# Performance work log

Measured on AMD Instinct MI355X. Metric: run time of the kernel, lower is better.

## Reference

```python
import jax, jax.numpy as jnp
import numpy as np

EPS = 1e-6


def softmax_kernel_transformation(data, is_query, projection_matrix):
    # data: [B,L,H,D], projection_matrix: [M,D]
    d = data.shape[-1]
    m = projection_matrix.shape[0]
    data_normalizer = 1.0 / jnp.sqrt(jnp.sqrt(jnp.float32(d)))
    data = data_normalizer * data
    ratio = 1.0 / jnp.sqrt(jnp.float32(m))
    data_dash = jnp.einsum('blhd,md->blhm', data, projection_matrix)
    diag_data = jnp.sum(jnp.square(data), axis=-1, keepdims=True) / 2.0  # [B,L,H,1]
    if is_query:
        stab = jnp.max(data_dash, axis=-1, keepdims=True)  # per-position max over M
    else:
        stab = jnp.max(data_dash, axis=(1, 3), keepdims=True)  # max over L and M
    return ratio * (jnp.exp(data_dash - diag_data - stab) + EPS)


def causal_linear_attention(qp, kp, v):
    # qp,kp: [L,B,H,M]; v: [L,B,H,D]. Sequential prefix-sum recurrence (FAVOR+ causal).
    B, H, M = qp.shape[1], qp.shape[2], qp.shape[3]
    D = v.shape[-1]
    kv0 = jnp.zeros((B, H, M, D), dtype=v.dtype)
    ks0 = jnp.zeros((B, H, M), dtype=kp.dtype)

    def step(carry, inp):
        kv_sum, k_sum = carry
        q_t, k_t, v_t = inp  # [B,H,M], [B,H,M], [B,H,D]
        kv_sum = kv_sum + jnp.einsum('bhm,bhd->bhmd', k_t, v_t)
        k_sum = k_sum + k_t
        num_t = jnp.einsum('bhmd,bhm->bhd', kv_sum, q_t)  # numerator row
        den_t = jnp.einsum('bhm,bhm->bh', q_t, k_sum)     # normalizer row
        return (kv_sum, k_sum), (num_t, den_t)

    (_, _), (num, den) = jax.lax.scan(step, (kv0, ks0), (qp, kp, v))
    return num, den  # [L,B,H,D], [L,B,H]


def favor_attention(query, key, value, projection_matrix):
    query_prime = softmax_kernel_transformation(query, True, projection_matrix)   # [B,L,H,M]
    key_prime = softmax_kernel_transformation(key, False, projection_matrix)      # [B,L,H,M]
    qp = jnp.transpose(query_prime, (1, 0, 2, 3))  # [L,B,H,M]
    kp = jnp.transpose(key_prime, (1, 0, 2, 3))
    v = jnp.transpose(value, (1, 0, 2, 3))         # [L,B,H,D]
    num, den = causal_linear_attention(qp, kp, v)
    av = jnp.transpose(num, (1, 0, 2, 3))          # [B,L,H,D]
    norm = jnp.transpose(den, (1, 0, 2))[..., None]  # [B,L,H,1]
    return av / norm


def setup_inputs() -> dict:
    B, L, H, D, M = 2, 2048, 8, 64, 128
    root = jax.random.key(0)
    kq, kk, kv, kp = jax.random.split(root, 4)
    return {
        'query': jax.random.normal(kq, (B, L, H, D), dtype=jnp.float32),
        'key': jax.random.normal(kk, (B, L, H, D), dtype=jnp.float32),
        'value': jax.random.normal(kv, (B, L, H, D), dtype=jnp.float32),
        'projection_matrix': jax.random.normal(kp, (M, D), dtype=jnp.float32),
    }


def reference(query, key, value, projection_matrix):
    return favor_attention(query, key, value, projection_matrix)
```

## Files before the change

kernel.cpp:

```cpp
#include <hip/hip_runtime.h>
#include <math.h>

typedef __attribute__((ext_vector_type(8))) short short8;
typedef __attribute__((ext_vector_type(4))) float f32x4;
typedef __attribute__((ext_vector_type(4))) unsigned short u16x4;

constexpr int B_ = 2, L_ = 2048, H_ = 8, D_ = 64, M_ = 128;
constexpr int T_ = 64;
constexpr int C_ = L_ / T_;
constexpr float DN_ = 0.35355339059327373f;
constexpr float RATIO_ = 0.08838834764831845f;
constexpr float EPSV_ = 1e-6f;
constexpr float REPS_ = RATIO_ * EPSV_;
constexpr float KEPS_ = 64.0f * REPS_;

constexpr int XQH_ = 0, XQL_ = 4608, XKH_ = 9216, XKL_ = 13824;
constexpr int PHO_ = 18432, PLO_ = 27648;
constexpr int QPST_ = 0, VTO_ = 9216, KPTO_ = 18432, KVSTO_ = 27648;

__device__ inline unsigned short f2bf(float x) {
  const unsigned u = __float_as_uint(x);
  return (unsigned short)((u + 0x7fffu + ((u >> 16) & 1u)) >> 16);
}
__device__ inline float bf2f(unsigned short h) {
  return __uint_as_float(((unsigned)h) << 16);
}

__global__ __launch_bounds__(256, 2) void feat_kernel(
    const float* __restrict__ q, const float* __restrict__ k,
    const float* __restrict__ P, const float* __restrict__ v,
    unsigned short* __restrict__ qp16, unsigned short* __restrict__ kp16,
    unsigned short* __restrict__ kvc16, float* __restrict__ ksc,
    unsigned short* __restrict__ vt16, float* __restrict__ blockmax,
    float* __restrict__ vsum) {
  __shared__ __align__(16) unsigned short sm[36864];
  __shared__ float diagq_s[T_];
  __shared__ float diagk_s[T_];
  __shared__ float wred_s[2][T_];
  __shared__ float red4_s[4];

  const int sub = blockIdx.x;
  const int c = sub % C_, bh = sub / C_;
  const int b = bh >> 3, h = bh & 7;
  const int tid = threadIdx.x;
  const int w = tid >> 6, lane = tid & 63;
  const int l15 = lane & 15, l16 = lane >> 4;
  const int rblk = (w >> 1) * 32, cblk = (w & 1) * 64;

  f32x4 vreg[4];
#pragma unroll
  for (int it = 0; it < 4; ++it) {
    const int i4 = tid + 256 * it;
    const int r = i4 >> 4, d0 = (i4 & 15) * 4;
    vreg[it] = *reinterpret_cast<const f32x4*>(
        &v[((size_t)(b * L_ + c * T_ + r) * H_ + h) * D_ + d0]);
  }

#define STAGE_X(xptr, XB, LB, dg)                                             \
  _Pragma("unroll") for (int it = 0; it < 4; ++it) {                          \
    const int i4 = tid + 256 * it;                                            \
    const int r = i4 >> 4, d0 = (i4 & 15) * 4;                                \
    f32x4 t4 = *reinterpret_cast<const f32x4*>(                               \
        &(xptr)[((size_t)(b * L_ + c * T_ + r) * H_ + h) * D_ + d0]);         \
    u16x4 hi, lo;                                                             \
    float sq = 0.f;                                                           \
    _Pragma("unroll") for (int j = 0; j < 4; ++j) {                           \
      const float xv = t4[j] * DN_;                                           \
      sq += xv * xv;                                                          \
      const unsigned short hb = f2bf(xv);                                     \
      hi[j] = hb;                                                             \
      lo[j] = f2bf(xv - bf2f(hb));                                            \
    }                                                                         \
    *reinterpret_cast<u16x4*>(&sm[(XB) + r * 72 + d0]) = hi;                  \
    *reinterpret_cast<u16x4*>(&sm[(LB) + r * 72 + d0]) = lo;                  \
    _Pragma("unroll") for (int off = 1; off < 16; off <<= 1)                  \
        sq += __shfl_xor(sq, off, 64);                                        \
    if ((tid & 15) == 0) (dg)[r] = sq;                                        \
  }

#define DASH_MFMA(accv, XB, LB)                                               \
  _Pragma("unroll") for (int kk = 0; kk < 2; ++kk) {                          \
    short8 ah[2], al[2], bh8[4], bl8[4];                                      \
    _Pragma("unroll") for (int ti = 0; ti < 2; ++ti) {                        \
      ah[ti] = *reinterpret_cast<const short8*>(                              \
          &sm[(XB) + (rblk + ti * 16 + l15) * 72 + kk * 32 + l16 * 8]);       \
      al[ti] = *reinterpret_cast<const short8*>(                              \
          &sm[(LB) + (rblk + ti * 16 + l15) * 72 + kk * 32 + l16 * 8]);       \
    }                                                                         \
    _Pragma("unroll") for (int tj = 0; tj < 4; ++tj) {                        \
      bh8[tj] = *reinterpret_cast<const short8*>(                             \
          &sm[PHO_ + (cblk + tj * 16 + l15) * 72 + kk * 32 + l16 * 8]);       \
      bl8[tj] = *reinterpret_cast<const short8*>(                             \
          &sm[PLO_ + (cblk + tj * 16 + l15) * 72 + kk * 32 + l16 * 8]);       \
    }                                                                         \
    _Pragma("unroll") for (int ti = 0; ti < 2; ++ti)                          \
        _Pragma("unroll") for (int tj = 0; tj < 4; ++tj) {                    \
      accv[ti][tj] = __builtin_amdgcn_mfma_f32_16x16x32_bf16(                 \
          al[ti], bh8[tj], accv[ti][tj], 0, 0, 0);                            \
      accv[ti][tj] = __builtin_amdgcn_mfma_f32_16x16x32_bf16(                 \
          ah[ti], bl8[tj], accv[ti][tj], 0, 0, 0);                            \
      accv[ti][tj] = __builtin_amdgcn_mfma_f32_16x16x32_bf16(                 \
          ah[ti], bh8[tj], accv[ti][tj], 0, 0, 0);                            \
    }                                                                         \
  }

  STAGE_X(q, XQH_, XQL_, diagq_s);
  STAGE_X(k, XKH_, XKL_, diagk_s);
  for (int i4 = tid; i4 < M_ * 16; i4 += 256) {
    const int m = i4 >> 4, d0 = (i4 & 15) * 4;
    const f32x4 t4 = *reinterpret_cast<const f32x4*>(&P[m * D_ + d0]);
    u16x4 hi, lo;
#pragma unroll
    for (int j = 0; j < 4; ++j) {
      hi[j] = f2bf(t4[j]);
      lo[j] = f2bf(t4[j] - bf2f(hi[j]));
    }
    *reinterpret_cast<u16x4*>(&sm[PHO_ + m * 72 + d0]) = hi;
    *reinterpret_cast<u16x4*>(&sm[PLO_ + m * 72 + d0]) = lo;
  }
  __syncthreads();

  f32x4 accq[2][4];
#pragma unroll
  for (int i = 0; i < 2; ++i)
#pragma unroll
    for (int j = 0; j < 4; ++j) accq[i][j] = {0.f, 0.f, 0.f, 0.f};
  DASH_MFMA(accq, XQH_, XQL_);

  {
    float rmax[2][4];
#pragma unroll
    for (int ti = 0; ti < 2; ++ti)
#pragma unroll
      for (int j = 0; j < 4; ++j) {
        float m0 = fmaxf(fmaxf(accq[ti][0][j], accq[ti][1][j]),
                         fmaxf(accq[ti][2][j], accq[ti][3][j]));
#pragma unroll
        for (int off = 1; off < 16; off <<= 1)
          m0 = fmaxf(m0, __shfl_xor(m0, off, 64));
        rmax[ti][j] = m0;
      }
    if (l15 == 0) {
#pragma unroll
      for (int ti = 0; ti < 2; ++ti)
#pragma unroll
        for (int j = 0; j < 4; ++j)
          wred_s[w & 1][rblk + ti * 16 + l16 * 4 + j] = rmax[ti][j];
    }
  }
  __syncthreads();

  f32x4 acck[2][4];
#pragma unroll
  for (int i = 0; i < 2; ++i)
#pragma unroll
    for (int j = 0; j < 4; ++j) acck[i][j] = {0.f, 0.f, 0.f, 0.f};
  DASH_MFMA(acck, XKH_, XKL_);
  {
    float bm = -INFINITY;
#pragma unroll
    for (int ti = 0; ti < 2; ++ti)
#pragma unroll
      for (int tj = 0; tj < 4; ++tj)
#pragma unroll
        for (int j = 0; j < 4; ++j) bm = fmaxf(bm, acck[ti][tj][j]);
#pragma unroll
    for (int off = 1; off < 64; off <<= 1)
      bm = fmaxf(bm, __shfl_xor(bm, off, 64));
    if (lane == 0) red4_s[w] = bm;
  }
#pragma unroll
  for (int ti = 0; ti < 2; ++ti)
#pragma unroll
    for (int j = 0; j < 4; ++j) {
      const int row = rblk + ti * 16 + l16 * 4 + j;
      const float sub2 =
          0.5f * diagq_s[row] + fmaxf(wred_s[0][row], wred_s[1][row]);
#pragma unroll
      for (int tj = 0; tj < 4; ++tj) {
        const int col = cblk + tj * 16 + l15;
        sm[QPST_ + row * 136 + col] =
            f2bf(RATIO_ * (expf(accq[ti][tj][j] - sub2) + EPSV_));
      }
    }
  __syncthreads();

  {
    unsigned short* outr = qp16 + ((size_t)bh * L_ + c * T_) * M_;
    for (int i8 = tid; i8 < T_ * 16; i8 += 256) {
      const int row = i8 >> 4, m0 = (i8 & 15) * 8;
      *reinterpret_cast<short8*>(&outr[row * M_ + m0]) =
          *reinterpret_cast<const short8*>(&sm[QPST_ + row * 136 + m0]);
    }
  }
  const float lmax =
      fmaxf(fmaxf(red4_s[0], red4_s[1]), fmaxf(red4_s[2], red4_s[3]));
  if (tid == 0) blockmax[sub] = lmax;

  {
    unsigned short* kpr = kp16 + ((size_t)bh * L_ + c * T_) * M_;
#pragma unroll
    for (int ti = 0; ti < 2; ++ti)
#pragma unroll
      for (int j = 0; j < 4; ++j) {
        const int row = rblk + ti * 16 + l16 * 4 + j;
        const float sub2 = 0.5f * diagk_s[row] + lmax;
#pragma unroll
        for (int tj = 0; tj < 4; ++tj) {
          const int col = cblk + tj * 16 + l15;
          const unsigned short us = f2bf(RATIO_ * expf(acck[ti][tj][j] - sub2));
          kpr[row * M_ + col] = us;
          sm[KPTO_ + col * 72 + row] = us;
        }
      }
  }
#pragma unroll
  for (int it = 0; it < 4; ++it) {
    const int i4 = tid + 256 * it;
    const int t = i4 >> 4, d0 = (i4 & 15) * 4;
#pragma unroll
    for (int j = 0; j < 4; ++j) sm[VTO_ + (d0 + j) * 72 + t] = f2bf(vreg[it][j]);
  }
  __syncthreads();

  {
    unsigned short* vg = vt16 + (size_t)(bh * C_ + c) * (D_ * T_);
    for (int i8 = tid; i8 < D_ * 8; i8 += 256) {
      const int d = i8 >> 3, t0 = (i8 & 7) * 8;
      *reinterpret_cast<short8*>(&vg[d * T_ + t0]) =
          *reinterpret_cast<const short8*>(&sm[VTO_ + d * 72 + t0]);
    }
  }
  if (tid < M_) {
    float s = 0.f;
#pragma unroll
    for (int t8 = 0; t8 < 8; ++t8) {
      const short8 h8 =
          *reinterpret_cast<const short8*>(&sm[KPTO_ + tid * 72 + t8 * 8]);
#pragma unroll
      for (int j = 0; j < 8; ++j) s += bf2f((unsigned short)h8[j]);
    }
    ksc[(size_t)(bh * C_ + c) * M_ + tid] = s;
  }
  if (tid >= 128 && tid < 128 + D_) {
    const int d = tid - 128;
    float s = 0.f;
#pragma unroll
    for (int t8 = 0; t8 < 8; ++t8) {
      const short8 h8 =
          *reinterpret_cast<const short8*>(&sm[VTO_ + d * 72 + t8 * 8]);
#pragma unroll
      for (int j = 0; j < 8; ++j) s += bf2f((unsigned short)h8[j]);
    }
    vsum[(size_t)(bh * C_ + c) * D_ + d] = s;
  }
  f32x4 acc2[2][4];
#pragma unroll
  for (int i = 0; i < 2; ++i)
#pragma unroll
    for (int j = 0; j < 4; ++j) acc2[i][j] = {0.f, 0.f, 0.f, 0.f};
#pragma unroll
  for (int kk = 0; kk < 2; ++kk) {
    short8 av[2], bv[4];
#pragma unroll
    for (int ti = 0; ti < 2; ++ti)
      av[ti] = *reinterpret_cast<const short8*>(
          &sm[VTO_ + (rblk + ti * 16 + l15) * 72 + kk * 32 + l16 * 8]);
#pragma unroll
    for (int tj = 0; tj < 4; ++tj)
      bv[tj] = *reinterpret_cast<const short8*>(
          &sm[KPTO_ + (cblk + tj * 16 + l15) * 72 + kk * 32 + l16 * 8]);
#pragma unroll
    for (int ti = 0; ti < 2; ++ti)
#pragma unroll
      for (int tj = 0; tj < 4; ++tj)
        acc2[ti][tj] = __builtin_amdgcn_mfma_f32_16x16x32_bf16(
            av[ti], bv[tj], acc2[ti][tj], 0, 0, 0);
  }
#pragma unroll
  for (int ti = 0; ti < 2; ++ti)
#pragma unroll
    for (int j = 0; j < 4; ++j) {
      const int row = rblk + ti * 16 + l16 * 4 + j;
#pragma unroll
      for (int tj = 0; tj < 4; ++tj) {
        const int col = cblk + tj * 16 + l15;
        sm[KVSTO_ + row * 136 + col] = f2bf(acc2[ti][tj][j]);
      }
    }
  __syncthreads();
  {
    unsigned short* ob = kvc16 + (size_t)(bh * C_ + c) * (M_ * D_);
    for (int i8 = tid; i8 < D_ * 16; i8 += 256) {
      const int d = i8 >> 4, m0 = (i8 & 15) * 8;
      *reinterpret_cast<short8*>(&ob[d * M_ + m0]) =
          *reinterpret_cast<const short8*>(&sm[KVSTO_ + d * 136 + m0]);
    }
  }
#undef STAGE_X
#undef DASH_MFMA
}

__global__ __launch_bounds__(256) void prefix_kernel(
    const unsigned short* __restrict__ kvc16,
    unsigned short* __restrict__ kvp16, float* __restrict__ ksc,
    const float* __restrict__ blockmax, const float* __restrict__ vsum) {
  __shared__ float bm_s[C_];
  __shared__ float sc_s[C_];
  __shared__ float vs_s[2][C_];
  const int bid = blockIdx.x;
  const int ej = bid & 31, bh = bid >> 5;
  if (threadIdx.x < C_) bm_s[threadIdx.x] = blockmax[bh * C_ + threadIdx.x];
  if (threadIdx.x >= 64 && threadIdx.x < 64 + 2 * C_) {
    const int t = threadIdx.x - 64;
    const int ld = t >> 5, cc = t & 31;
    vs_s[ld][cc] = vsum[(size_t)(bh * C_ + cc) * D_ + ej * 2 + ld];
  }
  __syncthreads();
  if (threadIdx.x < C_) {
    float km = -INFINITY;
#pragma unroll
    for (int cc = 0; cc < C_; ++cc) km = fmaxf(km, bm_s[cc]);
    sc_s[threadIdx.x] = expf(bm_s[threadIdx.x] - km);
  }
  __syncthreads();
  const int e = ej * 256 + threadIdx.x;
  const int dl = threadIdx.x >> 7;
  float vals[C_];
#pragma unroll
  for (int cc = 0; cc < C_; ++cc)
    vals[cc] = bf2f(kvc16[(size_t)(bh * C_ + cc) * (M_ * D_) + e]) * sc_s[cc] +
               REPS_ * vs_s[dl][cc];
  float run = 0.f;
#pragma unroll
  for (int cc = 0; cc < C_; ++cc) {
    const float t = vals[cc];
    vals[cc] = run;
    run += t;
  }
#pragma unroll
  for (int cc = 0; cc < C_; ++cc)
    kvp16[(size_t)(bh * C_ + cc) * (M_ * D_) + e] = f2bf(vals[cc]);
  if (ej == 0 && threadIdx.x < M_) {
    const int m = threadIdx.x;
    float ks[C_];
#pragma unroll
    for (int cc = 0; cc < C_; ++cc)
      ks[cc] = ksc[(size_t)(bh * C_ + cc) * M_ + m] * sc_s[cc] + KEPS_;
    float rs = 0.f;
#pragma unroll
    for (int cc = 0; cc < C_; ++cc) {
      const float t = ks[cc];
      ks[cc] = rs;
      rs += t;
    }
#pragma unroll
    for (int cc = 0; cc < C_; ++cc)
      ksc[(size_t)(bh * C_ + cc) * M_ + m] = ks[cc];
  }
}

__global__ __launch_bounds__(256, 3) void intra_kernel(
    const unsigned short* __restrict__ qp16,
    const unsigned short* __restrict__ kp16,
    const unsigned short* __restrict__ vt16,
    const unsigned short* __restrict__ kvp16, const float* __restrict__ ksp,
    const float* __restrict__ blockmax, float* __restrict__ out) {
  __shared__ __align__(16) unsigned short qp_s[T_][136];
  __shared__ __align__(16) unsigned short kp_s[T_][136];
  __shared__ __align__(16) unsigned short S_s[T_][72];
  __shared__ float ksp_s[M_];
  __shared__ float denp_s[4][T_];
  __shared__ float den_s[T_];
  __shared__ float qsum_s[T_];
  __shared__ float bm_s[C_];

  const int bid = blockIdx.x;
  const int c = bid % C_, bh = bid / C_;
  const int b = bh >> 3, h = bh & 7;
  const int tid = threadIdx.x;
  const int w = tid >> 6, lane = tid & 63;
  const int l15 = lane & 15, l16 = lane >> 4;
  const int dblk = (w & 1) * 32;

  const unsigned short* qpt = qp16 + ((size_t)bh * L_ + c * T_) * M_;
  const unsigned short* kpt = kp16 + ((size_t)bh * L_ + c * T_) * M_;
  const unsigned short* kvt = kvp16 + (size_t)(bh * C_ + c) * (M_ * D_);
  const unsigned short* vg = vt16 + (size_t)(bh * C_ + c) * (D_ * T_);

  short8 vtr[2][2], kvr[4][2];
#pragma unroll
  for (int kk = 0; kk < 2; ++kk)
#pragma unroll
    for (int tj = 0; tj < 2; ++tj)
      vtr[kk][tj] = *reinterpret_cast<const short8*>(
          &vg[(dblk + tj * 16 + l15) * T_ + kk * 32 + l16 * 8]);
#pragma unroll
  for (int kk = 0; kk < 4; ++kk)
#pragma unroll
    for (int tj = 0; tj < 2; ++tj)
      kvr[kk][tj] = *reinterpret_cast<const short8*>(
          &kvt[(dblk + tj * 16 + l15) * M_ + kk * 32 + l16 * 8]);

  if (tid < C_) bm_s[tid] = blockmax[bh * C_ + tid];
  for (int i8 = tid; i8 < T_ * 16; i8 += 256) {
    const int r = i8 >> 4, m0 = (i8 & 15) * 8;
    *reinterpret_cast<short8*>(&qp_s[r][m0]) =
        *reinterpret_cast<const short8*>(&qpt[r * M_ + m0]);
    *reinterpret_cast<short8*>(&kp_s[r][m0]) =
        *reinterpret_cast<const short8*>(&kpt[r * M_ + m0]);
  }
  if (tid < M_) ksp_s[tid] = ksp[(size_t)(bh * C_ + c) * M_ + tid];
  __syncthreads();

  {
    const int row = w * 16 + (lane >> 2), mseg = (lane & 3) * 32;
    float p = 0.f;
#pragma unroll
    for (int u = 0; u < 4; ++u) {
      const short8 h8 =
          *reinterpret_cast<const short8*>(&qp_s[row][mseg + u * 8]);
#pragma unroll
      for (int j = 0; j < 8; ++j) p += bf2f((unsigned short)h8[j]);
    }
    p += __shfl_xor(p, 1, 64);
    p += __shfl_xor(p, 2, 64);
    if ((lane & 3) == 0) qsum_s[row] = p;
  }
  __syncthreads();

  float km = -INFINITY;
#pragma unroll
  for (int cc = 0; cc < C_; ++cc) km = fmaxf(km, bm_s[cc]);
  const float sc = expf(bm_s[c] - km);

  const int rblk = (w >> 1) * 32, cblk = (w & 1) * 32;
  f32x4 Sacc[2][2];
#pragma unroll
  for (int i = 0; i < 2; ++i)
#pragma unroll
    for (int j = 0; j < 2; ++j) Sacc[i][j] = {0.f, 0.f, 0.f, 0.f};

#pragma unroll
  for (int kk = 0; kk < 4; ++kk) {
    short8 af[2], bf[2];
#pragma unroll
    for (int ti = 0; ti < 2; ++ti)
      af[ti] = *reinterpret_cast<const short8*>(
          &qp_s[rblk + ti * 16 + l15][kk * 32 + l16 * 8]);
#pragma unroll
    for (int tj = 0; tj < 2; ++tj)
      bf[tj] = *reinterpret_cast<const short8*>(
          &kp_s[cblk + tj * 16 + l15][kk * 32 + l16 * 8]);
#pragma unroll
    for (int ti = 0; ti < 2; ++ti)
#pragma unroll
      for (int tj = 0; tj < 2; ++tj)
        Sacc[ti][tj] = __builtin_amdgcn_mfma_f32_16x16x32_bf16(
            af[ti], bf[tj], Sacc[ti][tj], 0, 0, 0);
  }
#pragma unroll
  for (int ti = 0; ti < 2; ++ti)
#pragma unroll
    for (int tj = 0; tj < 2; ++tj)
#pragma unroll
      for (int j = 0; j < 4; ++j) {
        const int row = rblk + ti * 16 + l16 * 4 + j;
        const int col = cblk + tj * 16 + l15;
        const float add = REPS_ * qsum_s[row];
        const float sv = (col <= row) ? Sacc[ti][tj][j] * sc + add : 0.f;
        S_s[row][col] = f2bf(sv);
      }
  __syncthreads();

  {
    const int t = lane;
    float p = 0.f;
    if (w == 0) {
      for (int tp = 0; tp < 32; ++tp) p += bf2f(S_s[t][tp]);
    } else if (w == 1) {
      for (int tp = 32; tp < 64; ++tp) p += bf2f(S_s[t][tp]);
    } else if (w == 2) {
      for (int m = 0; m < 64; ++m) p += bf2f(qp_s[t][m]) * ksp_s[m];
    } else {
      for (int m = 64; m < 128; ++m) p += bf2f(qp_s[t][m]) * ksp_s[m];
    }
    denp_s[w][t] = p;
  }
  __syncthreads();
  if (tid < T_)
    den_s[tid] =
        denp_s[0][tid] + denp_s[1][tid] + denp_s[2][tid] + denp_s[3][tid];
  __syncthreads();

  f32x4 Nacc[2][2];
#pragma unroll
  for (int i = 0; i < 2; ++i)
#pragma unroll
    for (int j = 0; j < 2; ++j) Nacc[i][j] = {0.f, 0.f, 0.f, 0.f};

#pragma unroll
  for (int kk = 0; kk < 2; ++kk) {
    short8 af[2];
#pragma unroll
    for (int ti = 0; ti < 2; ++ti)
      af[ti] = *reinterpret_cast<const short8*>(
          &S_s[rblk + ti * 16 + l15][kk * 32 + l16 * 8]);
#pragma unroll
    for (int ti = 0; ti < 2; ++ti)
#pragma unroll
      for (int tj = 0; tj < 2; ++tj)
        Nacc[ti][tj] = __builtin_amdgcn_mfma_f32_16x16x32_bf16(
            af[ti], vtr[kk][tj], Nacc[ti][tj], 0, 0, 0);
  }
#pragma unroll
  for (int kk = 0; kk < 4; ++kk) {
    short8 af[2];
#pragma unroll
    for (int ti = 0; ti < 2; ++ti)
      af[ti] = *reinterpret_cast<const short8*>(
          &qp_s[rblk + ti * 16 + l15][kk * 32 + l16 * 8]);
#pragma unroll
    for (int ti = 0; ti < 2; ++ti)
#pragma unroll
      for (int tj = 0; tj < 2; ++tj)
        Nacc[ti][tj] = __builtin_amdgcn_mfma_f32_16x16x32_bf16(
            af[ti], kvr[kk][tj], Nacc[ti][tj], 0, 0, 0);
  }

#pragma unroll
  for (int ti = 0; ti < 2; ++ti)
#pragma unroll
    for (int j = 0; j < 4; ++j) {
      const int row = rblk + ti * 16 + l16 * 4 + j;
      const float r = 1.f / den_s[row];
      float* orow = out + ((size_t)(b * L_ + c * T_ + row) * H_ + h) * D_;
#pragma unroll
      for (int tj = 0; tj < 2; ++tj) {
        const int col = dblk + tj * 16 + l15;
        orow[col] = Nacc[ti][tj][j] * r;
      }
    }
}

extern "C" void kernel_launch(void* const* d_in, const int* in_sizes, int n_in,
                              void* d_out, int out_size, void* d_ws,
                              size_t ws_size, hipStream_t stream) {
  const float* q = (const float*)d_in[0];
  const float* k = (const float*)d_in[1];
  const float* v = (const float*)d_in[2];
  const float* P = (const float*)d_in[3];
  float* out = (float*)d_out;

  float* ws = (float*)d_ws;
  float* blockmax = ws;
  float* ksp = blockmax + 512;
  float* vsum = ksp + (size_t)B_ * H_ * C_ * M_;
  unsigned short* qp16 = (unsigned short*)(vsum + (size_t)B_ * H_ * C_ * D_);
  unsigned short* kp16 = qp16 + (size_t)B_ * H_ * L_ * M_;
  unsigned short* kvc16 = kp16 + (size_t)B_ * H_ * L_ * M_;
  unsigned short* kvp16 = kvc16 + (size_t)B_ * H_ * C_ * D_ * M_;
  unsigned short* vt16 = kvp16 + (size_t)B_ * H_ * C_ * D_ * M_;

  feat_kernel<<<B_ * H_ * C_, 256, 0, stream>>>(q, k, P, v, qp16, kp16, kvc16,
                                                ksp, vt16, blockmax, vsum);
  prefix_kernel<<<B_ * H_ * 32, 256, 0, stream>>>(kvc16, kvp16, ksp, blockmax,
                                                  vsum);
  intra_kernel<<<B_ * H_ * C_, 256, 0, stream>>>(qp16, kp16, vt16, kvp16, ksp,
                                                 blockmax, out);
}
```

Before: 43.76 us.

## Drop split-bf16 projection, shrink LDS, and merge Q/K feature phases

Replaces the three-MFMA hi/lo split-bf16 emulation of the fp32 projection with a single bf16 MFMA, which removes the lo staging buffers. LDS use drops enough to raise launch bounds to 3 blocks per CU. The Q and K projections are computed back to back with fewer barriers, and V staging moves earlier. The buffer regions now alias, so an extra barrier is added before KV storage. This cuts MFMA work and raises occupancy, but the projection loses precision: with exp of logits, bf16 rounding of q/k/P could push errors past tolerance.

```diff
diff --git a/kernel.cpp b/kernel.cpp
--- a/kernel.cpp
+++ b/kernel.cpp
@@ -14,9 +14,8 @@
 constexpr float REPS_ = RATIO_ * EPSV_;
 constexpr float KEPS_ = 64.0f * REPS_;
 
-constexpr int XQH_ = 0, XQL_ = 4608, XKH_ = 9216, XKL_ = 13824;
-constexpr int PHO_ = 18432, PLO_ = 27648;
-constexpr int QPST_ = 0, VTO_ = 9216, KPTO_ = 18432, KVSTO_ = 27648;
+constexpr int XQ_ = 0, XK_ = 4608, PHO_ = 9216, VTO_ = 18432;
+constexpr int QPST_ = 0, KPTO_ = 9216, KVSTO_ = 0;
 
 __device__ inline unsigned short f2bf(float x) {
   const unsigned u = __float_as_uint(x);
@@ -26,14 +25,14 @@
   return __uint_as_float(((unsigned)h) << 16);
 }
 
-__global__ __launch_bounds__(256, 2) void feat_kernel(
+__global__ __launch_bounds__(256, 3) void feat_kernel(
     const float* __restrict__ q, const float* __restrict__ k,
     const float* __restrict__ P, const float* __restrict__ v,
     unsigned short* __restrict__ qp16, unsigned short* __restrict__ kp16,
     unsigned short* __restrict__ kvc16, float* __restrict__ ksc,
     unsigned short* __restrict__ vt16, float* __restrict__ blockmax,
     float* __restrict__ vsum) {
-  __shared__ __align__(16) unsigned short sm[36864];
+  __shared__ __align__(16) unsigned short sm[23040];
   __shared__ float diagq_s[T_];
   __shared__ float diagk_s[T_];
   __shared__ float wred_s[2][T_];
@@ -47,86 +46,71 @@
   const int l15 = lane & 15, l16 = lane >> 4;
   const int rblk = (w >> 1) * 32, cblk = (w & 1) * 64;
 
-  f32x4 vreg[4];
-#pragma unroll
-  for (int it = 0; it < 4; ++it) {
-    const int i4 = tid + 256 * it;
-    const int r = i4 >> 4, d0 = (i4 & 15) * 4;
-    vreg[it] = *reinterpret_cast<const f32x4*>(
-        &v[((size_t)(b * L_ + c * T_ + r) * H_ + h) * D_ + d0]);
-  }
-
-#define STAGE_X(xptr, XB, LB, dg)                                             \
+#define STAGE_X(xptr, XB, dg)                                                 \
   _Pragma("unroll") for (int it = 0; it < 4; ++it) {                          \
     const int i4 = tid + 256 * it;                                            \
     const int r = i4 >> 4, d0 = (i4 & 15) * 4;                                \
     f32x4 t4 = *reinterpret_cast<const f32x4*>(                               \
         &(xptr)[((size_t)(b * L_ + c * T_ + r) * H_ + h) * D_ + d0]);         \
-    u16x4 hi, lo;                                                             \
+    u16x4 hi;                                                                 \
     float sq = 0.f;                                                           \
     _Pragma("unroll") for (int j = 0; j < 4; ++j) {                           \
       const float xv = t4[j] * DN_;                                           \
       sq += xv * xv;                                                          \
-      const unsigned short hb = f2bf(xv);                                     \
-      hi[j] = hb;                                                             \
-      lo[j] = f2bf(xv - bf2f(hb));                                            \
+      hi[j] = f2bf(xv);                                                       \
     }                                                                         \
     *reinterpret_cast<u16x4*>(&sm[(XB) + r * 72 + d0]) = hi;                  \
-    *reinterpret_cast<u16x4*>(&sm[(LB) + r * 72 + d0]) = lo;                  \
     _Pragma("unroll") for (int off = 1; off < 16; off <<= 1)                  \
         sq += __shfl_xor(sq, off, 64);                                        \
     if ((tid & 15) == 0) (dg)[r] = sq;                                        \
   }
 
-#define DASH_MFMA(accv, XB, LB)                                               \
+#define DASH_MFMA(accv, XB)                                                   \
   _Pragma("unroll") for (int kk = 0; kk < 2; ++kk) {                          \
-    short8 ah[2], al[2], bh8[4], bl8[4];                                      \
-    _Pragma("unroll") for (int ti = 0; ti < 2; ++ti) {                        \
+    short8 ah[2], bh8[4];                                                     \
+    _Pragma("unroll") for (int ti = 0; ti < 2; ++ti)                          \
       ah[ti] = *reinterpret_cast<const short8*>(                              \
           &sm[(XB) + (rblk + ti * 16 + l15) * 72 + kk * 32 + l16 * 8]);       \
-      al[ti] = *reinterpret_cast<const short8*>(                              \
-          &sm[(LB) + (rblk + ti * 16 + l15) * 72 + kk * 32 + l16 * 8]);       \
-    }                                                                         \
-    _Pragma("unroll") for (int tj = 0; tj < 4; ++tj) {                        \
+    _Pragma("unroll") for (int tj = 0; tj < 4; ++tj)                          \
       bh8[tj] = *reinterpret_cast<const short8*>(                             \
           &sm[PHO_ + (cblk + tj * 16 + l15) * 72 + kk * 32 + l16 * 8]);       \
-      bl8[tj] = *reinterpret_cast<const short8*>(                             \
-          &sm[PLO_ + (cblk + tj * 16 + l15) * 72 + kk * 32 + l16 * 8]);       \
-    }                                                                         \
     _Pragma("unroll") for (int ti = 0; ti < 2; ++ti)                          \
-        _Pragma("unroll") for (int tj = 0; tj < 4; ++tj) {                    \
-      accv[ti][tj] = __builtin_amdgcn_mfma_f32_16x16x32_bf16(                 \
-          al[ti], bh8[tj], accv[ti][tj], 0, 0, 0);                            \
-      accv[ti][tj] = __builtin_amdgcn_mfma_f32_16x16x32_bf16(                 \
-          ah[ti], bl8[tj], accv[ti][tj], 0, 0, 0);                            \
-      accv[ti][tj] = __builtin_amdgcn_mfma_f32_16x16x32_bf16(                 \
-          ah[ti], bh8[tj], accv[ti][tj], 0, 0, 0);                            \
-    }                                                                         \
-  }
-
-  STAGE_X(q, XQH_, XQL_, diagq_s);
-  STAGE_X(k, XKH_, XKL_, diagk_s);
+        _Pragma("unroll") for (int tj = 0; tj < 4; ++tj)                      \
+            accv[ti][tj] = __builtin_amdgcn_mfma_f32_16x16x32_bf16(           \
+                ah[ti], bh8[tj], accv[ti][tj], 0, 0, 0);                      \
+  }
+
+  STAGE_X(q, XQ_, diagq_s);
+  STAGE_X(k, XK_, diagk_s);
   for (int i4 = tid; i4 < M_ * 16; i4 += 256) {
     const int m = i4 >> 4, d0 = (i4 & 15) * 4;
     const f32x4 t4 = *reinterpret_cast<const f32x4*>(&P[m * D_ + d0]);
-    u16x4 hi, lo;
+    u16x4 hi;
+#pragma unroll
+    for (int j = 0; j < 4; ++j) hi[j] = f2bf(t4[j]);
+    *reinterpret_cast<u16x4*>(&sm[PHO_ + m * 72 + d0]) = hi;
+  }
+#pragma unroll
+  for (int it = 0; it < 4; ++it) {
+    const int i4 = tid + 256 * it;
+    const int t = i4 >> 4, d0 = (i4 & 15) * 4;
+    const f32x4 t4 = *reinterpret_cast<const f32x4*>(
+        &v[((size_t)(b * L_ + c * T_ + t) * H_ + h) * D_ + d0]);
+#pragma unroll
+    for (int j = 0; j < 4; ++j) sm[VTO_ + (d0 + j) * 72 + t] = f2bf(t4[j]);
+  }
+  __syncthreads();
+
+  f32x4 accq[2][4], acck[2][4];
+#pragma unroll
+  for (int i = 0; i < 2; ++i)
 #pragma unroll
     for (int j = 0; j < 4; ++j) {
-      hi[j] = f2bf(t4[j]);
-      lo[j] = f2bf(t4[j] - bf2f(hi[j]));
-    }
-    *reinterpret_cast<u16x4*>(&sm[PHO_ + m * 72 + d0]) = hi;
-    *reinterpret_cast<u16x4*>(&sm[PLO_ + m * 72 + d0]) = lo;
-  }
-  __syncthreads();
-
-  f32x4 accq[2][4];
-#pragma unroll
-  for (int i = 0; i < 2; ++i)
-#pragma unroll
-    for (int j = 0; j < 4; ++j) accq[i][j] = {0.f, 0.f, 0.f, 0.f};
-  DASH_MFMA(accq, XQH_, XQL_);
-
+      accq[i][j] = {0.f, 0.f, 0.f, 0.f};
+      acck[i][j] = {0.f, 0.f, 0.f, 0.f};
+    }
+  DASH_MFMA(accq, XQ_);
+  DASH_MFMA(acck, XK_);
   {
     float rmax[2][4];
 #pragma unroll
@@ -148,14 +132,6 @@
           wred_s[w & 1][rblk + ti * 16 + l16 * 4 + j] = rmax[ti][j];
     }
   }
-  __syncthreads();
-
-  f32x4 acck[2][4];
-#pragma unroll
-  for (int i = 0; i < 2; ++i)
-#pragma unroll
-    for (int j = 0; j < 4; ++j) acck[i][j] = {0.f, 0.f, 0.f, 0.f};
-  DASH_MFMA(acck, XKH_, XKL_);
   {
     float bm = -INFINITY;
 #pragma unroll
@@ -169,6 +145,11 @@
       bm = fmaxf(bm, __shfl_xor(bm, off, 64));
     if (lane == 0) red4_s[w] = bm;
   }
+  __syncthreads();
+
+  const float lmax =
+      fmaxf(fmaxf(red4_s[0], red4_s[1]), fmaxf(red4_s[2], red4_s[3]));
+  if (tid == 0) blockmax[sub] = lmax;
 #pragma unroll
   for (int ti = 0; ti < 2; ++ti)
 #pragma unroll
@@ -183,20 +164,6 @@
             f2bf(RATIO_ * (expf(accq[ti][tj][j] - sub2) + EPSV_));
       }
     }
-  __syncthreads();
-
-  {
-    unsigned short* outr = qp16 + ((size_t)bh * L_ + c * T_) * M_;
-    for (int i8 = tid; i8 < T_ * 16; i8 += 256) {
-      const int row = i8 >> 4, m0 = (i8 & 15) * 8;
-      *reinterpret_cast<short8*>(&outr[row * M_ + m0]) =
-          *reinterpret_cast<const short8*>(&sm[QPST_ + row * 136 + m0]);
-    }
-  }
-  const float lmax =
-      fmaxf(fmaxf(red4_s[0], red4_s[1]), fmaxf(red4_s[2], red4_s[3]));
-  if (tid == 0) blockmax[sub] = lmax;
-
   {
     unsigned short* kpr = kp16 + ((size_t)bh * L_ + c * T_) * M_;
 #pragma unroll
@@ -214,16 +181,15 @@
         }
       }
   }
-#pragma unroll
-  for (int it = 0; it < 4; ++it) {
-    const int i4 = tid + 256 * it;
-    const int t = i4 >> 4, d0 = (i4 & 15) * 4;
-#pragma unroll
-    for (int j = 0; j < 4; ++j) sm[VTO_ + (d0 + j) * 72 + t] = f2bf(vreg[it][j]);
-  }
-  __syncthreads();
-
-  {
+  __syncthreads();
+
+  {
+    unsigned short* outr = qp16 + ((size_t)bh * L_ + c * T_) * M_;
+    for (int i8 = tid; i8 < T_ * 16; i8 += 256) {
+      const int row = i8 >> 4, m0 = (i8 & 15) * 8;
+      *reinterpret_cast<short8*>(&outr[row * M_ + m0]) =
+          *reinterpret_cast<const short8*>(&sm[QPST_ + row * 136 + m0]);
+    }
     unsigned short* vg = vt16 + (size_t)(bh * C_ + c) * (D_ * T_);
     for (int i8 = tid; i8 < D_ * 8; i8 += 256) {
       const int d = i8 >> 3, t0 = (i8 & 7) * 8;
@@ -277,6 +243,7 @@
         acc2[ti][tj] = __builtin_amdgcn_mfma_f32_16x16x32_bf16(
             av[ti], bv[tj], acc2[ti][tj], 0, 0, 0);
   }
+  __syncthreads();
 #pragma unroll
   for (int ti = 0; ti < 2; ++ti)
 #pragma unroll
```

Result: faster. 41.61 us (-4.9%).
